# Kernel optimization log

Hardware: AMD Instinct MI355X
Metric: run time of the kernel (lower is better)

## Reference

```python
import jax, jax.numpy as jnp
import numpy as np

N, D, C = 4096, 512, 128
TOPK = 12  # rank-0 hard neg + up to 11 fallback ranks (torch loop breaks at loop_cnt>=10 -> max rank 11)


def setup_inputs() -> dict:
    key = jax.random.key(0)
    k1, k2, k3, k4, k5 = jax.random.split(key, 5)
    return {
        "inputs": jax.random.normal(k1, (N, D), jnp.float32),
        "prediction": jax.random.normal(k2, (N, C), jnp.float32),
        "targets": jax.random.randint(k3, (N,), 0, C),
        "true_targets": jax.random.randint(k4, (N,), 0, C),
        "prob": jax.random.uniform(k5, (N,), jnp.float32),
        "threshold": jnp.float32(0.5),
    }


def _gumbel_argmax(key, mask):
    # uniform random choice over True entries of each row (Gumbel-max trick)
    g = jax.random.gumbel(key, mask.shape, jnp.float32)
    return jnp.argmax(jnp.where(mask, g, -jnp.inf), axis=1)


def reference(inputs, prediction, targets, true_targets, prob, threshold):
    margin = jnp.float32(0.3)
    n = inputs.shape[0]
    rows = jnp.arange(n)
    # pairwise euclidean distance: ||xi||^2 + ||xj||^2 - 2 xi.xj, clamp+sqrt
    sq = jnp.sum(inputs * inputs, axis=1)
    d2 = sq[:, None] + sq[None, :] - 2.0 * (inputs @ inputs.T)
    dist = jnp.sqrt(jnp.clip(d2, 1e-12))  # [n, n]

    eye = jnp.eye(n, dtype=bool)
    same = targets[:, None] == targets[None, :]
    is_neg = ~same
    conf = prob >= threshold  # is_confident per anchor

    key = jax.random.key(42)
    kp, kp2 = jax.random.split(key)

    # random positive (!= i) and hardest negative per row
    ap_idx = _gumbel_argmax(kp, same & ~eye)
    neg_dist = jnp.where(is_neg, dist, jnp.inf)
    an_idx = jnp.argmin(neg_dist, axis=1)

    ap0 = dist[rows, ap_idx]
    an0 = dist[rows, an_idx]
    pos_conf = prob[ap_idx] >= threshold
    neg_conf = prob[an_idx] >= threshold
    # false-negative test: hard neg predicted as anchor's (noisy) label
    is_fn = jnp.argmax(prediction[an_idx], axis=1) == targets

    # case B (pos conf, neg unconf, FN): walk ranked negs for first confident one (ranks 1..11)
    nv, ni = jax.lax.top_k(-neg_dist, TOPK)  # smallest TOPK neg distances
    cand_conf = prob[ni] >= threshold
    tail = cand_conf[:, 1:]
    found = jnp.any(tail, axis=1)
    r = jnp.where(found, 1 + jnp.argmax(tail, axis=1), TOPK - 1)
    an_B = dist[rows, ni[rows, r]]

    # cases C / D-notFN: resample a confident positive (!= i); fallback to original pos
    conf_pos = same & ~eye & (prob >= threshold)[None, :]
    new_pos = jnp.where(jnp.any(conf_pos, axis=1), _gumbel_argmax(kp2, conf_pos), ap_idx)
    ap_new = dist[rows, new_pos]

    caseB = pos_conf & ~neg_conf & is_fn
    swap = (~pos_conf) & (neg_conf | ~is_fn)  # case C or case D-notFN
    inverse = (~pos_conf) & (~neg_conf) & is_fn

    half = (ap0 + an0) * 0.5
    ap = jnp.where(caseB, half, jnp.where(swap, ap_new, ap0))
    an = jnp.where(caseB, an_B, jnp.where(swap, half, an0))

    row_loss = jnp.where(inverse,
                         jax.nn.relu(an - ap + margin),
                         jax.nn.relu(ap - an + margin))
    cnt = jnp.sum(conf)
    loss = jnp.sum(jnp.where(conf, row_loss, 0.0)) / jnp.maximum(cnt, 1).astype(jnp.float32)
    correct = jnp.sum((an >= ap) & conf)
    return loss, correct
```

## Files before the change

### kernel.cpp

```cpp
#include <hip/hip_runtime.h>
#include <stdint.h>
#include <math.h>

#define N_ 4096
#define D_ 512
#define C_ 128
#define MAXC 256

typedef __attribute__((ext_vector_type(8))) short bf16x8;
typedef __attribute__((ext_vector_type(4))) float f32x4;

__host__ __device__ __forceinline__ uint32_t rotl32_(uint32_t x, int d) {
  return (x << d) | (x >> (32 - d));
}
__host__ __device__ inline void tf2x32(uint32_t k0, uint32_t k1,
                                       uint32_t x0, uint32_t x1,
                                       uint32_t& y0, uint32_t& y1) {
  const uint32_t k2 = k0 ^ k1 ^ 0x1BD11BDAu;
#define TF_R(rr) { x0 += x1; x1 = rotl32_(x1, rr); x1 ^= x0; }
  x0 += k0; x1 += k1;
  TF_R(13) TF_R(15) TF_R(26) TF_R(6)
  x0 += k1; x1 += k2 + 1u;
  TF_R(17) TF_R(29) TF_R(16) TF_R(24)
  x0 += k2; x1 += k0 + 2u;
  TF_R(13) TF_R(15) TF_R(26) TF_R(6)
  x0 += k0; x1 += k1 + 3u;
  TF_R(17) TF_R(29) TF_R(16) TF_R(24)
  x0 += k1; x1 += k2 + 4u;
  TF_R(13) TF_R(15) TF_R(26) TF_R(6)
  x0 += k2; x1 += k0 + 5u;
#undef TF_R
  y0 = x0; y1 = x1;
}

__device__ __forceinline__ float gumbel_ij(uint32_t k0, uint32_t k1, uint32_t m) {
  uint32_t y0, y1;
  tf2x32(k0, k1, 0u, m, y0, y1);
  uint32_t bits = y0 ^ y1;
  uint32_t vb = (bits >> 9) | 0x3f800000u;
  float f = __uint_as_float(vb) - 1.0f;
  float u = (f == 0.0f) ? 1.1754943508222875e-38f : f;
  return -logf(-logf(u));
}

__device__ __forceinline__ unsigned short f2bf(float x) {
  unsigned int b = __float_as_uint(x);
  b += 0x7fffu + ((b >> 16) & 1u);
  return (unsigned short)(b >> 16);
}
__device__ __forceinline__ float bf2f(unsigned short u) {
  return __uint_as_float(((unsigned int)u) << 16);
}

__device__ __forceinline__ void gll16(const void* g, void* lds) {
  __builtin_amdgcn_global_load_lds(
      (const __attribute__((address_space(1))) unsigned int*)g,
      (__attribute__((address_space(3))) unsigned int*)lds, 16, 0, 0);
}

__global__ void zero_k(float* __restrict__ accum, int* __restrict__ ccnt) {
  int t = threadIdx.x;
  if (t == 0) {
    accum[0] = 0.0f;
    ((unsigned*)accum)[1] = 0u;
    ((unsigned*)accum)[2] = 0u;
  }
  if (t < C_) ccnt[t] = 0;
}

__global__ __launch_bounds__(64) void prep_k(const float* __restrict__ inputs,
                                             const float* __restrict__ pred,
                                             const int* __restrict__ targets,
                                             float* __restrict__ sq,
                                             int* __restrict__ pam,
                                             int* __restrict__ ccnt,
                                             int* __restrict__ clist,
                                             unsigned short* __restrict__ XH,
                                             unsigned short* __restrict__ XL,
                                             int do_split, int do_list) {
  int i = blockIdx.x;
  int lane = threadIdx.x;
  const float4* rp = (const float4*)(inputs + (size_t)i * D_);
  float s = 0.0f;
#pragma unroll
  for (int q = 0; q < 2; ++q) {
    float4 v = rp[lane + 64 * q];
    s += v.x * v.x + v.y * v.y + v.z * v.z + v.w * v.w;
    if (do_split) {
      unsigned short h0 = f2bf(v.x), h1 = f2bf(v.y), h2 = f2bf(v.z), h3 = f2bf(v.w);
      unsigned short g0 = f2bf(v.x - bf2f(h0)), g1 = f2bf(v.y - bf2f(h1));
      unsigned short g2 = f2bf(v.z - bf2f(h2)), g3 = f2bf(v.w - bf2f(h3));
      uint2 hp, lp;
      hp.x = (unsigned)h0 | ((unsigned)h1 << 16); hp.y = (unsigned)h2 | ((unsigned)h3 << 16);
      lp.x = (unsigned)g0 | ((unsigned)g1 << 16); lp.y = (unsigned)g2 | ((unsigned)g3 << 16);
      *(uint2*)&XH[(size_t)i * D_ + 4 * (lane + 64 * q)] = hp;
      *(uint2*)&XL[(size_t)i * D_ + 4 * (lane + 64 * q)] = lp;
    }
  }
#pragma unroll
  for (int off = 32; off; off >>= 1) s += __shfl_down(s, off);
  if (lane == 0) sq[i] = s;

  float v0 = pred[(size_t)i * C_ + lane];
  float v1 = pred[(size_t)i * C_ + 64 + lane];
  float bv; int bi;
  if (v1 > v0) { bv = v1; bi = lane + 64; } else { bv = v0; bi = lane; }
#pragma unroll
  for (int off = 32; off; off >>= 1) {
    float ov = __shfl_down(bv, off);
    int oi = __shfl_down(bi, off);
    if (ov > bv || (ov == bv && oi < bi)) { bv = ov; bi = oi; }
  }
  if (lane == 0) {
    pam[i] = bi;
    if (do_list) {
      int t = targets[i];
      int p = atomicAdd(&ccnt[t], 1);
      if (p < MAXC) clist[t * MAXC + p] = i;
    }
  }
}

__global__ __launch_bounds__(256, 2) void bigk3_k(const unsigned short* __restrict__ XH,
                                                  const unsigned short* __restrict__ XL,
                                                  const int* __restrict__ targets,
                                                  const float* __restrict__ sq,
                                                  float* __restrict__ pD,
                                                  int* __restrict__ pI) {
  __shared__ float U[8448];
  __shared__ float sqc[512];
  __shared__ int tcs[512];
  __shared__ float sqr[64];
  __shared__ int trs[64];

  const int tid = threadIdx.x, w = tid >> 6, l = tid & 63;
  const int rb = blockIdx.x >> 3, sl = blockIdx.x & 7;
  const int rbase = rb * 64, cbase0 = sl * 512;

  sqc[tid] = sq[cbase0 + tid]; sqc[tid + 256] = sq[cbase0 + 256 + tid];
  tcs[tid] = targets[cbase0 + tid]; tcs[tid + 256] = targets[cbase0 + 256 + tid];
  if (tid < 64) { sqr[tid] = sq[rbase + tid]; trs[tid] = targets[rbase + tid]; }

  const int lr = l & 15, lk = (l >> 4) * 8;
  const unsigned short* aH[4]; const unsigned short* aL[4];
  const unsigned short* bH[8]; const unsigned short* bL[8];
#pragma unroll
  for (int rt = 0; rt < 4; ++rt) {
    size_t o = (size_t)(rbase + rt * 16 + lr) * D_ + lk;
    aH[rt] = XH + o; aL[rt] = XL + o;
  }
#pragma unroll
  for (int c = 0; c < 8; ++c) {
    size_t o = (size_t)(cbase0 + (w * 8 + c) * 16 + lr) * D_ + lk;
    bH[c] = XH + o; bL[c] = XL + o;
  }

  f32x4 acc[4][8];
#pragma unroll
  for (int rt = 0; rt < 4; ++rt)
#pragma unroll
    for (int c = 0; c < 8; ++c) acc[rt][c] = (f32x4){0.f, 0.f, 0.f, 0.f};

  for (int kc = 0; kc < 16; ++kc) {
    const int kb = kc * 32;
    bf16x8 ah[4], al_[4];
#pragma unroll
    for (int rt = 0; rt < 4; ++rt) {
      ah[rt] = *(const bf16x8*)(aH[rt] + kb);
      al_[rt] = *(const bf16x8*)(aL[rt] + kb);
    }
#pragma unroll
    for (int c = 0; c < 8; ++c) {
      bf16x8 bh = *(const bf16x8*)(bH[c] + kb);
      bf16x8 bl = *(const bf16x8*)(bL[c] + kb);
#pragma unroll
      for (int rt = 0; rt < 4; ++rt) {
        acc[rt][c] = __builtin_amdgcn_mfma_f32_16x16x32_bf16(ah[rt], bh, acc[rt][c], 0, 0, 0);
        acc[rt][c] = __builtin_amdgcn_mfma_f32_16x16x32_bf16(ah[rt], bl, acc[rt][c], 0, 0, 0);
        acc[rt][c] = __builtin_amdgcn_mfma_f32_16x16x32_bf16(al_[rt], bh, acc[rt][c], 0, 0, 0);
      }
    }
  }

  float* Dl = U;
  float dl[12]; int il[12];
#pragma unroll
  for (int q = 0; q < 12; ++q) { dl[q] = INFINITY; il[q] = 0; }
  const int srow = tid >> 2, scq = tid & 3;
  const int orow = (l >> 4) * 4;

  for (int g = 0; g < 4; ++g) {
    __syncthreads();
    if (w == g) {
#pragma unroll
      for (int rt = 0; rt < 4; ++rt)
#pragma unroll
        for (int c = 0; c < 8; ++c)
#pragma unroll
          for (int r = 0; r < 4; ++r) {
            int row = rt * 16 + orow + r;
            int cl = c * 16 + lr;
            float d2 = sqr[row] + sqc[g * 128 + cl] - 2.0f * acc[rt][c][r];
            float d = (trs[row] == tcs[g * 128 + cl]) ? INFINITY : sqrtf(fmaxf(d2, 1e-12f));
            Dl[row * 132 + cl] = d;
          }
    }
    __syncthreads();
    for (int q = 0; q < 32; ++q) {
      float d = Dl[srow * 132 + scq + 4 * q];
      if (d < dl[11]) {
        int col = cbase0 + g * 128 + scq + 4 * q;
        bool placed = false;
#pragma unroll
        for (int t = 11; t >= 1; --t) {
          if (!placed) {
            if (dl[t - 1] > d) { dl[t] = dl[t - 1]; il[t] = il[t - 1]; }
            else { dl[t] = d; il[t] = col; placed = true; }
          }
        }
        if (!placed) { dl[0] = d; il[0] = col; }
      }
    }
  }

  __syncthreads();
  float* MD = U;
  int* MI = (int*)(U + 3072);
#pragma unroll
  for (int q = 0; q < 12; ++q) { MD[tid * 12 + q] = dl[q]; MI[tid * 12 + q] = il[q]; }
  __syncthreads();
  if ((tid & 3) == 0) {
    int row = tid >> 2;
    int grow = rbase + row;
    float* outD = pD + ((size_t)grow * 8 + sl) * 12;
    int* outI = pI + ((size_t)grow * 8 + sl) * 12;
    int p0 = 0, p1 = 0, p2 = 0, p3 = 0;
    for (int o = 0; o < 12; ++o) {
      float bd = INFINITY; int bi = 0x7fffffff; int bc = 0;
      if (p0 < 12) { float d = MD[(row * 4 + 0) * 12 + p0]; int ix = MI[(row * 4 + 0) * 12 + p0]; if (d < bd || (d == bd && ix < bi)) { bd = d; bi = ix; bc = 0; } }
      if (p1 < 12) { float d = MD[(row * 4 + 1) * 12 + p1]; int ix = MI[(row * 4 + 1) * 12 + p1]; if (d < bd || (d == bd && ix < bi)) { bd = d; bi = ix; bc = 1; } }
      if (p2 < 12) { float d = MD[(row * 4 + 2) * 12 + p2]; int ix = MI[(row * 4 + 2) * 12 + p2]; if (d < bd || (d == bd && ix < bi)) { bd = d; bi = ix; bc = 2; } }
      if (p3 < 12) { float d = MD[(row * 4 + 3) * 12 + p3]; int ix = MI[(row * 4 + 3) * 12 + p3]; if (d < bd || (d == bd && ix < bi)) { bd = d; bi = ix; bc = 3; } }
      outD[o] = bd; outI[o] = bi;
      if (bc == 0) p0++; else if (bc == 1) p1++; else if (bc == 2) p2++; else p3++;
    }
  }
}

__global__ __launch_bounds__(256, 2) void bigk_k(const float* __restrict__ inputs,
                                                 const int* __restrict__ targets,
                                                 const float* __restrict__ sq,
                                                 float* __restrict__ pD,
                                                 int* __restrict__ pI) {
  __shared__ float U[10496];
  __shared__ float sqc[256];
  __shared__ int tcs[256];
  __shared__ float sqr[64];
  __shared__ int trs[64];

  float* Al = U;
  float* Bl = U + 2176;
  float* Dl = U;
  float* MD = U;
  int* MI = (int*)(U + 3072);

  const int tid = threadIdx.x;
  const int rb = blockIdx.x >> 3, sl = blockIdx.x & 7;
  const int rbase = rb * 64, cbase0 = sl * 512;

  if (tid < 64) { sqr[tid] = sq[rbase + tid]; trs[tid] = targets[rbase + tid]; }

  float dl[12]; int il[12];
#pragma unroll
  for (int q = 0; q < 12; ++q) { dl[q] = INFINITY; il[q] = 0; }

  const int w = tid >> 6, lane = tid & 63;
  const int rg = lane >> 3, cg = lane & 7;
  const int r0 = rg * 8, c0l = w * 64 + cg * 8;
  const int srow = tid >> 2, scq = tid & 3;

  for (int ci = 0; ci < 2; ++ci) {
    const int cbase = cbase0 + ci * 256;
    __syncthreads();
    sqc[tid] = sq[cbase + tid];
    tcs[tid] = targets[cbase + tid];

    float acc[8][8];
#pragma unroll
    for (int a = 0; a < 8; ++a)
#pragma unroll
      for (int b = 0; b < 8; ++b) acc[a][b] = 0.0f;

    for (int kc = 0; kc < 16; ++kc) {
      const int kb = kc * 32;
      __syncthreads();
#pragma unroll
      for (int q = 0; q < 2; ++q) {
        int idx = tid + 256 * q;
        int row = idx >> 3, kq = idx & 7;
        float4 v = *(const float4*)(inputs + (size_t)(rbase + row) * D_ + kb + kq * 4);
        Al[(4 * kq + 0) * 68 + row] = v.x;
        Al[(4 * kq + 1) * 68 + row] = v.y;
        Al[(4 * kq + 2) * 68 + row] = v.z;
        Al[(4 * kq + 3) * 68 + row] = v.w;
      }
#pragma unroll
      for (int q = 0; q < 8; ++q) {
        int idx = tid + 256 * q;
        int col = idx >> 3, kq = idx & 7;
        float4 v = *(const float4*)(inputs + (size_t)(cbase + col) * D_ + kb + kq * 4);
        Bl[(4 * kq + 0) * 260 + col] = v.x;
        Bl[(4 * kq + 1) * 260 + col] = v.y;
        Bl[(4 * kq + 2) * 260 + col] = v.z;
        Bl[(4 * kq + 3) * 260 + col] = v.w;
      }
      __syncthreads();
#pragma unroll 4
      for (int k = 0; k < 32; ++k) {
        float4 a0 = *(const float4*)&Al[k * 68 + r0];
        float4 a1 = *(const float4*)&Al[k * 68 + r0 + 4];
        float4 b0 = *(const float4*)&Bl[k * 260 + c0l];
        float4 b1 = *(const float4*)&Bl[k * 260 + c0l + 4];
        float a_[8] = {a0.x, a0.y, a0.z, a0.w, a1.x, a1.y, a1.z, a1.w};
        float b_[8] = {b0.x, b0.y, b0.z, b0.w, b1.x, b1.y, b1.z, b1.w};
#pragma unroll
        for (int ii = 0; ii < 8; ++ii)
#pragma unroll
          for (int jj = 0; jj < 8; ++jj)
            acc[ii][jj] = fmaf(a_[ii], b_[jj], acc[ii][jj]);
      }
    }

    for (int h = 0; h < 2; ++h) {
      __syncthreads();
#pragma unroll
      for (int i = 0; i < 8; ++i) {
        float si = sqr[r0 + i];
        int ti_ = trs[r0 + i];
#pragma unroll
        for (int jj = 0; jj < 4; ++jj) {
          int j = 4 * h + jj;
          float d2 = si + sqc[c0l + j] - 2.0f * acc[i][j];
          float d = (ti_ == tcs[c0l + j]) ? INFINITY : sqrtf(fmaxf(d2, 1e-12f));
          Dl[(r0 + i) * 129 + (w * 32 + cg * 4 + jj)] = d;
        }
      }
      __syncthreads();
      for (int q = 0; q < 32; ++q) {
        float d = Dl[srow * 129 + scq * 32 + q];
        if (d < dl[11]) {
          int u = scq * 32 + q;
          int col = cbase + ((u >> 5) << 6) + (((u >> 2) & 7) << 3) + (h << 2) + (u & 3);
          bool placed = false;
#pragma unroll
          for (int t = 11; t >= 1; --t) {
            if (!placed) {
              if (dl[t - 1] > d) { dl[t] = dl[t - 1]; il[t] = il[t - 1]; }
              else { dl[t] = d; il[t] = col; placed = true; }
            }
          }
          if (!placed) { dl[0] = d; il[0] = col; }
        }
      }
    }
  }

  __syncthreads();
#pragma unroll
  for (int q = 0; q < 12; ++q) { MD[tid * 12 + q] = dl[q]; MI[tid * 12 + q] = il[q]; }
  __syncthreads();
  if ((tid & 3) == 0) {
    int row = tid >> 2;
    int grow = rbase + row;
    float* outD = pD + ((size_t)grow * 8 + sl) * 12;
    int* outI = pI + ((size_t)grow * 8 + sl) * 12;
    int p0 = 0, p1 = 0, p2 = 0, p3 = 0;
    for (int o = 0; o < 12; ++o) {
      float bd = INFINITY; int bi = 0x7fffffff; int bc = 0;
      if (p0 < 12) { float d = MD[(row * 4 + 0) * 12 + p0]; int ix = MI[(row * 4 + 0) * 12 + p0]; if (d < bd || (d == bd && ix < bi)) { bd = d; bi = ix; bc = 0; } }
      if (p1 < 12) { float d = MD[(row * 4 + 1) * 12 + p1]; int ix = MI[(row * 4 + 1) * 12 + p1]; if (d < bd || (d == bd && ix < bi)) { bd = d; bi = ix; bc = 1; } }
      if (p2 < 12) { float d = MD[(row * 4 + 2) * 12 + p2]; int ix = MI[(row * 4 + 2) * 12 + p2]; if (d < bd || (d == bd && ix < bi)) { bd = d; bi = ix; bc = 2; } }
      if (p3 < 12) { float d = MD[(row * 4 + 3) * 12 + p3]; int ix = MI[(row * 4 + 3) * 12 + p3]; if (d < bd || (d == bd && ix < bi)) { bd = d; bi = ix; bc = 3; } }
      outD[o] = bd; outI[o] = bi;
      if (bc == 0) p0++; else if (bc == 1) p1++; else if (bc == 2) p2++; else p3++;
    }
  }
}

__device__ __forceinline__ float wdist2(float4 xi0, float4 xi1,
                                        const float* __restrict__ inputs,
                                        const float* __restrict__ sq,
                                        int i, int j, int lane) {
  const float4* b = (const float4*)(inputs + (size_t)j * D_);
  float4 y0 = b[lane], y1 = b[lane + 64];
  float s = xi0.x * y0.x + xi0.y * y0.y + xi0.z * y0.z + xi0.w * y0.w +
            xi1.x * y1.x + xi1.y * y1.y + xi1.z * y1.z + xi1.w * y1.w;
#pragma unroll
  for (int off = 32; off; off >>= 1) s += __shfl_xor(s, off);
  float d2 = sq[i] + sq[j] - 2.0f * s;
  return sqrtf(fmaxf(d2, 1e-12f));
}

__global__ __launch_bounds__(256) void finalize_k(const float* __restrict__ inputs,
                                                  const int* __restrict__ targets,
                                                  const float* __restrict__ prob,
                                                  const float* __restrict__ thr_p,
                                                  const float* __restrict__ sq,
                                                  const int* __restrict__ pam,
                                                  const float* __restrict__ pD,
                                                  const int* __restrict__ pI,
                                                  const int* __restrict__ ccnt,
                                                  const int* __restrict__ clist,
                                                  float* __restrict__ accum,
                                                  uint32_t kp0, uint32_t kp1,
                                                  uint32_t kq0, uint32_t kq1,
                                                  int use_list) {
  const int wid = threadIdx.x >> 6, lane = threadIdx.x & 63;
  const int i = blockIdx.x * 4 + wid;
  const float thr = *thr_p;
  const int ti = targets[i];

  float g1 = -INFINITY; int i1 = 0;
  float g2 = -INFINITY; int i2 = 0;
  int f2 = 0;
  if (use_list) {
    int cnt = ccnt[ti]; if (cnt > MAXC) cnt = MAXC;
    const int* lst = clist + (size_t)ti * MAXC;
    for (int base = 0; base < cnt; base += 64) {
      int idx = base + lane;
      if (idx < cnt) {
        int j = lst[idx];
        if (j != i) {
          uint32_t m = ((uint32_t)i << 12) | (uint32_t)j;
          float g = gumbel_ij(kp0, kp1, m);
          if (g > g1 || (g == g1 && j < i1)) { g1 = g; i1 = j; }
          if (prob[j] >= thr) {
            float gg = gumbel_ij(kq0, kq1, m);
            if (gg > g2 || (gg == g2 && j < i2)) { g2 = gg; i2 = j; }
            f2 = 1;
          }
        }
      }
    }
  } else {
    for (int j = lane; j < N_; j += 64) {
      if (targets[j] == ti && j != i) {
        uint32_t m = ((uint32_t)i << 12) | (uint32_t)j;
        float g = gumbel_ij(kp0, kp1, m);
        if (g > g1 || (g == g1 && j < i1)) { g1 = g; i1 = j; }
        if (prob[j] >= thr) {
          float gg = gumbel_ij(kq0, kq1, m);
          if (gg > g2 || (gg == g2 && j < i2)) { g2 = gg; i2 = j; }
          f2 = 1;
        }
      }
    }
  }
#pragma unroll
  for (int off = 32; off; off >>= 1) {
    float og = __shfl_xor(g1, off); int oi = __shfl_xor(i1, off);
    if (og > g1 || (og == g1 && oi < i1)) { g1 = og; i1 = oi; }
    float oh = __shfl_xor(g2, off); int oj = __shfl_xor(i2, off);
    if (oh > g2 || (oh == g2 && oj < i2)) { g2 = oh; i2 = oj; }
  }
  f2 = __any(f2);
  const int ap_idx = i1;
  const int new_pos = f2 ? i2 : ap_idx;

  const float4* arow = (const float4*)(inputs + (size_t)i * D_);
  float4 xi0 = arow[lane], xi1 = arow[lane + 64];
  const float ap0 = wdist2(xi0, xi1, inputs, sq, i, ap_idx, lane);
  const float ap_new = wdist2(xi0, xi1, inputs, sq, i, new_pos, lane);

  const float* rowD = pD + (size_t)i * 96;
  const int* rowI = pI + (size_t)i * 96;
  int ci_[12];
  {
    int p0 = 0, p1 = 0, p2 = 0, p3 = 0, p4 = 0, p5 = 0, p6 = 0, p7 = 0;
#pragma unroll
    for (int o = 0; o < 12; ++o) {
      float bd = INFINITY; int bi = 0x7fffffff; int bs = 0;
#define HEADQ(s, ps) if (ps < 12) { float d = rowD[(s) * 12 + ps]; int ix = rowI[(s) * 12 + ps]; if (d < bd || (d == bd && ix < bi)) { bd = d; bi = ix; bs = (s); } }
      HEADQ(0, p0) HEADQ(1, p1) HEADQ(2, p2) HEADQ(3, p3)
      HEADQ(4, p4) HEADQ(5, p5) HEADQ(6, p6) HEADQ(7, p7)
#undef HEADQ
      ci_[o] = bi;
      if (bs == 0) p0++; else if (bs == 1) p1++; else if (bs == 2) p2++; else if (bs == 3) p3++;
      else if (bs == 4) p4++; else if (bs == 5) p5++; else if (bs == 6) p6++; else p7++;
    }
  }
  float de[12];
#pragma unroll
  for (int o = 0; o < 12; ++o) de[o] = wdist2(xi0, xi1, inputs, sq, i, ci_[o], lane);

  float an0 = de[0]; int an_idx = ci_[0]; int minpos = 0;
#pragma unroll
  for (int o = 1; o < 12; ++o)
    if (de[o] < an0 || (de[o] == an0 && ci_[o] < an_idx)) { an0 = de[o]; an_idx = ci_[o]; minpos = o; }
  float anB = INFINITY; int anBi = 0x7fffffff; bool fB = false;
#pragma unroll
  for (int o = 0; o < 12; ++o) {
    if (o != minpos) {
      bool cf = prob[ci_[o]] >= thr;
      if (cf && (de[o] < anB || (de[o] == anB && ci_[o] < anBi))) { anB = de[o]; anBi = ci_[o]; fB = true; }
    }
  }
  if (!fB) {
    anB = de[0]; anBi = ci_[0];
#pragma unroll
    for (int o = 1; o < 12; ++o)
      if (de[o] > anB || (de[o] == anB && ci_[o] > anBi)) { anB = de[o]; anBi = ci_[o]; }
  }
  const float an_B = anB;

  if (lane == 0) {
    bool neg_conf = prob[an_idx] >= thr;
    bool pos_conf = prob[ap_idx] >= thr;
    bool is_fn = (pam[an_idx] == ti);
    bool caseB = pos_conf && !neg_conf && is_fn;
    bool swap_ = !pos_conf && (neg_conf || !is_fn);
    bool inverse = !pos_conf && !neg_conf && is_fn;
    float half = 0.5f * (ap0 + an0);
    float ap = caseB ? half : (swap_ ? ap_new : ap0);
    float an = caseB ? an_B : (swap_ ? half : an0);
    const float margin = 0.3f;
    float rl = inverse ? fmaxf(an - ap + margin, 0.0f) : fmaxf(ap - an + margin, 0.0f);
    bool conf_i = prob[i] >= thr;
    if (conf_i) {
      atomicAdd(&accum[0], rl);
      atomicAdd(((unsigned*)accum) + 2, 1u);
      if (an >= ap) atomicAdd(((unsigned*)accum) + 1, 1u);
    }
  }
}

__global__ void writeout_k(const float* __restrict__ accum, float* __restrict__ out) {
  unsigned correct = ((const unsigned*)accum)[1];
  unsigned cnt = ((const unsigned*)accum)[2];
  out[0] = accum[0] / fmaxf((float)cnt, 1.0f);
  out[1] = (float)correct;
}

extern "C" void kernel_launch(void* const* d_in, const int* in_sizes, int n_in,
                              void* d_out, int out_size, void* d_ws, size_t ws_size,
                              hipStream_t stream) {
  const float* inputs = (const float*)d_in[0];
  const float* pred = (const float*)d_in[1];
  const int* targets = (const int*)d_in[2];
  const float* prob = (const float*)d_in[4];
  const float* thr = (const float*)d_in[5];
  float* out = (float*)d_out;

  float* sq = (float*)d_ws;
  int* pam = (int*)d_ws + N_;
  float* pD = (float*)d_ws + 2 * N_;
  int* pI = (int*)d_ws + 2 * N_ + N_ * 96;
  float* accum = (float*)d_ws + 2 * N_ + 2 * (N_ * 96);
  int* ccnt = (int*)accum + 16;
  int* clist = ccnt + C_;
  const size_t base_f = (size_t)(2 * N_ + 2 * (N_ * 96) + 16 + C_ + C_ * MAXC);
  const size_t split_off = ((base_f * 4 + 15) / 16) * 16;
  unsigned short* XH = (unsigned short*)((char*)d_ws + split_off);
  unsigned short* XL = XH + (size_t)N_ * D_;
  const size_t need = split_off + (size_t)2 * N_ * D_ * 2;
  const int use_v2 = (ws_size >= need) ? 1 : 0;

  uint32_t kp0, kp1, kq0, kq1;
  tf2x32(0u, 42u, 0u, 0u, kp0, kp1);
  tf2x32(0u, 42u, 0u, 1u, kq0, kq1);

  zero_k<<<dim3(1), dim3(128), 0, stream>>>(accum, ccnt);
  prep_k<<<dim3(N_), dim3(64), 0, stream>>>(inputs, pred, targets, sq, pam, ccnt, clist,
                                            XH, XL, use_v2, use_v2);
  if (use_v2)
    bigk3_k<<<dim3(512), dim3(256), 0, stream>>>(XH, XL, targets, sq, pD, pI);
  else
    bigk_k<<<dim3(512), dim3(256), 0, stream>>>(inputs, targets, sq, pD, pI);
  finalize_k<<<dim3(N_ / 4), dim3(256), 0, stream>>>(inputs, targets, prob, thr, sq, pam,
                                                     pD, pI, ccnt, clist, accum,
                                                     kp0, kp1, kq0, kq1, use_v2);
  writeout_k<<<dim3(1), dim3(1), 0, stream>>>(accum, out);
}
```

Measured before the change: 403.9 us.

## Store bf16 split operands in MFMA-fragment-tiled layout for coalesced loads

```diff
diff --git a/kernel.cpp b/kernel.cpp
--- a/kernel.cpp
+++ b/kernel.cpp
@@ -52,12 +52,6 @@
   return __uint_as_float(((unsigned int)u) << 16);
 }
 
-__device__ __forceinline__ void gll16(const void* g, void* lds) {
-  __builtin_amdgcn_global_load_lds(
-      (const __attribute__((address_space(1))) unsigned int*)g,
-      (__attribute__((address_space(3))) unsigned int*)lds, 16, 0, 0);
-}
-
 __global__ void zero_k(float* __restrict__ accum, int* __restrict__ ccnt) {
   int t = threadIdx.x;
   if (t == 0) {
@@ -93,8 +87,11 @@
       uint2 hp, lp;
       hp.x = (unsigned)h0 | ((unsigned)h1 << 16); hp.y = (unsigned)h2 | ((unsigned)h3 << 16);
       lp.x = (unsigned)g0 | ((unsigned)g1 << 16); lp.y = (unsigned)g2 | ((unsigned)g3 << 16);
-      *(uint2*)&XH[(size_t)i * D_ + 4 * (lane + 64 * q)] = hp;
-      *(uint2*)&XL[(size_t)i * D_ + 4 * (lane + 64 * q)] = lp;
+      size_t blk = ((size_t)(i >> 4) * 16 + ((lane >> 3) + 8 * q)) * 512;
+      int lf = (i & 15) + 16 * ((lane & 7) >> 1);
+      int j0 = 4 * (lane & 1);
+      *(uint2*)&XH[blk + lf * 8 + j0] = hp;
+      *(uint2*)&XL[blk + lf * 8 + j0] = lp;
     }
   }
 #pragma unroll
@@ -121,7 +118,7 @@
   }
 }
 
-__global__ __launch_bounds__(256, 2) void bigk3_k(const unsigned short* __restrict__ XH,
+__global__ __launch_bounds__(256, 2) void bigk4_k(const unsigned short* __restrict__ XH,
                                                   const unsigned short* __restrict__ XL,
                                                   const int* __restrict__ targets,
                                                   const float* __restrict__ sq,
@@ -141,19 +138,12 @@
   tcs[tid] = targets[cbase0 + tid]; tcs[tid + 256] = targets[cbase0 + 256 + tid];
   if (tid < 64) { sqr[tid] = sq[rbase + tid]; trs[tid] = targets[rbase + tid]; }
 
-  const int lr = l & 15, lk = (l >> 4) * 8;
-  const unsigned short* aH[4]; const unsigned short* aL[4];
-  const unsigned short* bH[8]; const unsigned short* bL[8];
-#pragma unroll
-  for (int rt = 0; rt < 4; ++rt) {
-    size_t o = (size_t)(rbase + rt * 16 + lr) * D_ + lk;
-    aH[rt] = XH + o; aL[rt] = XL + o;
-  }
-#pragma unroll
-  for (int c = 0; c < 8; ++c) {
-    size_t o = (size_t)(cbase0 + (w * 8 + c) * 16 + lr) * D_ + lk;
-    bH[c] = XH + o; bL[c] = XL + o;
-  }
+  const int lo = l * 8;
+  size_t ta[4], tb[8];
+#pragma unroll
+  for (int rt = 0; rt < 4; ++rt) ta[rt] = (size_t)((rbase >> 4) + rt) * 8192;
+#pragma unroll
+  for (int c = 0; c < 8; ++c) tb[c] = (size_t)((cbase0 >> 4) + w * 8 + c) * 8192;
 
   f32x4 acc[4][8];
 #pragma unroll
@@ -162,17 +152,17 @@
     for (int c = 0; c < 8; ++c) acc[rt][c] = (f32x4){0.f, 0.f, 0.f, 0.f};
 
   for (int kc = 0; kc < 16; ++kc) {
-    const int kb = kc * 32;
+    const int off = kc * 512 + lo;
     bf16x8 ah[4], al_[4];
 #pragma unroll
     for (int rt = 0; rt < 4; ++rt) {
-      ah[rt] = *(const bf16x8*)(aH[rt] + kb);
-      al_[rt] = *(const bf16x8*)(aL[rt] + kb);
+      ah[rt] = *(const bf16x8*)(XH + ta[rt] + off);
+      al_[rt] = *(const bf16x8*)(XL + ta[rt] + off);
     }
 #pragma unroll
     for (int c = 0; c < 8; ++c) {
-      bf16x8 bh = *(const bf16x8*)(bH[c] + kb);
-      bf16x8 bl = *(const bf16x8*)(bL[c] + kb);
+      bf16x8 bh = *(const bf16x8*)(XH + tb[c] + off);
+      bf16x8 bl = *(const bf16x8*)(XL + tb[c] + off);
 #pragma unroll
       for (int rt = 0; rt < 4; ++rt) {
         acc[rt][c] = __builtin_amdgcn_mfma_f32_16x16x32_bf16(ah[rt], bh, acc[rt][c], 0, 0, 0);
@@ -188,6 +178,7 @@
   for (int q = 0; q < 12; ++q) { dl[q] = INFINITY; il[q] = 0; }
   const int srow = tid >> 2, scq = tid & 3;
   const int orow = (l >> 4) * 4;
+  const int lr = l & 15;
 
   for (int g = 0; g < 4; ++g) {
     __syncthreads();
@@ -573,7 +564,7 @@
   prep_k<<<dim3(N_), dim3(64), 0, stream>>>(inputs, pred, targets, sq, pam, ccnt, clist,
                                             XH, XL, use_v2, use_v2);
   if (use_v2)
-    bigk3_k<<<dim3(512), dim3(256), 0, stream>>>(XH, XL, targets, sq, pD, pI);
+    bigk4_k<<<dim3(512), dim3(256), 0, stream>>>(XH, XL, targets, sq, pD, pI);
   else
     bigk_k<<<dim3(512), dim3(256), 0, stream>>>(inputs, targets, sq, pD, pI);
   finalize_k<<<dim3(N_ / 4), dim3(256), 0, stream>>>(inputs, targets, prob, thr, sq, pam,
```

Measured after the change: 344.3 us. -14.8%, faster.
